# Kernel tuning notes

Measured on AMD Instinct MI355X. Metric: run time of the kernel, lower is better.

The kernel has to match this reference:

```python
import jax, jax.numpy as jnp
import numpy as np

IN_F = 1024
OUT_F = 1024
R = 16
NUM_USERS = 10000
NUM_ITEMS = 10000
BATCH = 4096
SCALING = 32.0 / 16.0  # lora_alpha / r


def setup_inputs() -> dict:
    key = jax.random.key(0)
    ks = jax.random.split(key, 9)
    return {
        "x": jax.random.normal(ks[0], (BATCH, IN_F), dtype=jnp.float32),
        "user_indices": jax.random.randint(ks[1], (BATCH,), 0, NUM_USERS, dtype=jnp.int32),
        "item_indices": jax.random.randint(ks[2], (BATCH,), 0, NUM_ITEMS, dtype=jnp.int32),
        "W_base": jax.random.normal(ks[3], (OUT_F, IN_F), dtype=jnp.float32) * 0.02,
        "b_base": jax.random.normal(ks[4], (OUT_F,), dtype=jnp.float32) * 0.02,
        "A": jax.random.normal(ks[5], (R, IN_F), dtype=jnp.float32) * 0.02,
        "B_user": jax.random.normal(ks[6], (NUM_USERS, OUT_F, R), dtype=jnp.float32) * 0.02,
        "B_item": jax.random.normal(ks[7], (NUM_ITEMS, OUT_F, R), dtype=jnp.float32) * 0.02,
        "W_common": jax.random.normal(ks[8], (OUT_F, R), dtype=jnp.float32) * 0.02,
    }


def reference(x, user_indices, item_indices, W_base, b_base, A, B_user, B_item, W_common):
    # base linear: [B, out]
    base = x @ W_base.T + b_base
    # lora_A (dropout p=0 -> identity): [B, r]
    a = x @ A.T
    # gather per-row LoRA-B matrices: [B, out, r]
    Bu = B_user[user_indices]
    Bi = B_item[item_indices]
    # batched low-rank matmuls + shared common projection
    user_part = jnp.einsum("bor,br->bo", Bu, a)
    item_part = jnp.einsum("bor,br->bo", Bi, a)
    common_part = a @ W_common.T
    return base + SCALING * (user_part + item_part + common_part)
```

## Files before the change

### kernel.cpp

```cpp
#include <hip/hip_runtime.h>
#include <hip/hip_bf16.h>
#include <cstdint>
#include <cstddef>

typedef __attribute__((ext_vector_type(8))) __bf16 bf16x8;
typedef __attribute__((ext_vector_type(4))) __bf16 bf16x4;
typedef __attribute__((ext_vector_type(4))) float f32x4;

#define BATCH 4096
#define IN_FEAT 1024
#define OUT_FEAT 1024
#define RNK 16
#define SCALE 2.0f

__global__ __launch_bounds__(256) void prep_kernel(
    const float* __restrict__ x, const float* __restrict__ A,
    const float* __restrict__ W,
    float* __restrict__ a_out, __bf16* __restrict__ x_bf,
    __bf16* __restrict__ w_bf)
{
    __shared__ float xs[IN_FEAT];
    const int b = blockIdx.x;
    const int t = threadIdx.x;

    if (b < OUT_FEAT) {
        const float4 wv = *reinterpret_cast<const float4*>(&W[(size_t)b * IN_FEAT + t * 4]);
        bf16x4 hw;
        hw[0] = (__bf16)wv.x; hw[1] = (__bf16)wv.y;
        hw[2] = (__bf16)wv.z; hw[3] = (__bf16)wv.w;
        *reinterpret_cast<bf16x4*>(&w_bf[(size_t)b * IN_FEAT + t * 4]) = hw;
    }

    const float4 v = *reinterpret_cast<const float4*>(&x[(size_t)b * IN_FEAT + t * 4]);
    xs[t * 4 + 0] = v.x; xs[t * 4 + 1] = v.y;
    xs[t * 4 + 2] = v.z; xs[t * 4 + 3] = v.w;
    bf16x4 h;
    h[0] = (__bf16)v.x; h[1] = (__bf16)v.y; h[2] = (__bf16)v.z; h[3] = (__bf16)v.w;
    *reinterpret_cast<bf16x4*>(&x_bf[(size_t)b * IN_FEAT + t * 4]) = h;
    __syncthreads();

    const int r = t >> 4;
    const int l16 = t & 15;
    const float* __restrict__ Ar = &A[r * IN_FEAT];
    float s = 0.f;
    #pragma unroll 8
    for (int j = 0; j < IN_FEAT / 16; ++j) {
        const int k = l16 + 16 * j;
        s += xs[k] * Ar[k];
    }
    s += __shfl_xor(s, 8);
    s += __shfl_xor(s, 4);
    s += __shfl_xor(s, 2);
    s += __shfl_xor(s, 1);
    if (l16 == 0) a_out[b * RNK + r] = s;
}

#define BM 64
#define BN 64
#define BK 64
#define LDK 72
#define CWS 20

__global__ __launch_bounds__(256) void fused_kernel(
    const __bf16* __restrict__ x_bf, const __bf16* __restrict__ w_bf,
    const float* __restrict__ a_buf,
    const int* __restrict__ uidx, const int* __restrict__ iidx,
    const float* __restrict__ b_base,
    const float* __restrict__ B_user, const float* __restrict__ B_item,
    const float* __restrict__ W_common,
    float* __restrict__ out)
{
    __shared__ __align__(16) __bf16 xs[BM * LDK];
    __shared__ __align__(16) __bf16 wsh[BN * LDK];
    __shared__ __align__(16) float a_s[BM * RNK];
    __shared__ __align__(16) float cw_s[BN * CWS];
    __shared__ float b_s[BN];
    __shared__ int u_s[BM];
    __shared__ int i_s[BM];

    const int t = threadIdx.x;

    const int bid = blockIdx.y * gridDim.x + blockIdx.x;
    const int nid = (bid & 7) * 128 + (bid >> 3);
    const int o0 = (nid & 15) * BN;
    const int b0 = (nid >> 4) * BM;

    if (t < BM) {
        u_s[t] = uidx[b0 + t];
        i_s[t] = iidx[b0 + t];
    }
    if (t < BN) b_s[t] = b_base[o0 + t];
    *reinterpret_cast<float4*>(&a_s[t * 4]) =
        *reinterpret_cast<const float4*>(&a_buf[(size_t)b0 * RNK + t * 4]);
    {
        const int row = t >> 2, col = (t & 3) * 4;
        const float4 v = *reinterpret_cast<const float4*>(
            &W_common[(size_t)(o0 + row) * RNK + col]);
        *reinterpret_cast<float4*>(&cw_s[row * CWS + col]) = v;
    }

    const int w  = t >> 6;
    const int wr = w >> 1;
    const int wc = w & 1;
    const int l  = t & 63;
    const int lr = l & 15;
    const int lg = l >> 4;

    const int srow  = t >> 2;
    const int skoff = (t & 3) * 16;

    f32x4 acc[2][2] = {};

    #pragma unroll
    for (int kt = 0; kt < IN_FEAT / BK; ++kt) {
        __syncthreads();
        {
            const uint4* g = reinterpret_cast<const uint4*>(
                &x_bf[(size_t)(b0 + srow) * IN_FEAT + kt * BK + skoff]);
            uint4 v0 = g[0], v1 = g[1];
            *reinterpret_cast<uint4*>(&xs[srow * LDK + skoff]) = v0;
            *reinterpret_cast<uint4*>(&xs[srow * LDK + skoff + 8]) = v1;
            const uint4* gw = reinterpret_cast<const uint4*>(
                &w_bf[(size_t)(o0 + srow) * IN_FEAT + kt * BK + skoff]);
            uint4 w0 = gw[0], w1 = gw[1];
            *reinterpret_cast<uint4*>(&wsh[srow * LDK + skoff]) = w0;
            *reinterpret_cast<uint4*>(&wsh[srow * LDK + skoff + 8]) = w1;
        }

        {
            const int nn = kt >> 3;
            const int mm = (kt >> 2) & 1;
            const int ii = kt & 3;
            const int ol = wc * 32 + nn * 16 + lr;
            const int o  = o0 + ol;
            const int bl = wr * 32 + mm * 16 + lg * 4 + ii;
            const size_t u  = (size_t)u_s[bl];
            const size_t iv = (size_t)i_s[bl];
            const float4* bu = reinterpret_cast<const float4*>(
                &B_user[(u * OUT_FEAT + (size_t)o) * RNK]);
            const float4* bi = reinterpret_cast<const float4*>(
                &B_item[(iv * OUT_FEAT + (size_t)o) * RNK]);
            const float4* av4 = reinterpret_cast<const float4*>(&a_s[bl * RNK]);
            const float4* cw4 = reinterpret_cast<const float4*>(&cw_s[ol * CWS]);
            float lora = 0.f;
            #pragma unroll
            for (int q = 0; q < 4; ++q) {
                const float4 cu = bu[q], ci = bi[q], aa = av4[q], cw = cw4[q];
                lora += (cu.x + ci.x + cw.x) * aa.x + (cu.y + ci.y + cw.y) * aa.y
                      + (cu.z + ci.z + cw.z) * aa.z + (cu.w + ci.w + cw.w) * aa.w;
            }
            acc[mm][nn][ii] += b_s[ol] + SCALE * lora;
        }
        __syncthreads();

        #pragma unroll
        for (int kk = 0; kk < BK; kk += 32) {
            bf16x8 af0 = *reinterpret_cast<const bf16x8*>(&xs[(wr * 32 + 0 * 16 + lr) * LDK + kk + lg * 8]);
            bf16x8 af1 = *reinterpret_cast<const bf16x8*>(&xs[(wr * 32 + 1 * 16 + lr) * LDK + kk + lg * 8]);
            bf16x8 bf0 = *reinterpret_cast<const bf16x8*>(&wsh[(wc * 32 + 0 * 16 + lr) * LDK + kk + lg * 8]);
            bf16x8 bf1 = *reinterpret_cast<const bf16x8*>(&wsh[(wc * 32 + 1 * 16 + lr) * LDK + kk + lg * 8]);
            acc[0][0] = __builtin_amdgcn_mfma_f32_16x16x32_bf16(af0, bf0, acc[0][0], 0, 0, 0);
            acc[0][1] = __builtin_amdgcn_mfma_f32_16x16x32_bf16(af0, bf1, acc[0][1], 0, 0, 0);
            acc[1][0] = __builtin_amdgcn_mfma_f32_16x16x32_bf16(af1, bf0, acc[1][0], 0, 0, 0);
            acc[1][1] = __builtin_amdgcn_mfma_f32_16x16x32_bf16(af1, bf1, acc[1][1], 0, 0, 0);
        }
    }

    #pragma unroll
    for (int n = 0; n < 2; ++n) {
        const int o = o0 + wc * 32 + n * 16 + lr;
        #pragma unroll
        for (int m = 0; m < 2; ++m) {
            #pragma unroll
            for (int i = 0; i < 4; ++i) {
                const int bl = wr * 32 + m * 16 + lg * 4 + i;
                out[(size_t)(b0 + bl) * OUT_FEAT + o] = acc[m][n][i];
            }
        }
    }
}

extern "C" void kernel_launch(void* const* d_in, const int* in_sizes, int n_in,
                              void* d_out, int out_size, void* d_ws, size_t ws_size,
                              hipStream_t stream) {
    const float* x        = (const float*)d_in[0];
    const int*   uidx     = (const int*)d_in[1];
    const int*   iidx     = (const int*)d_in[2];
    const float* W_base   = (const float*)d_in[3];
    const float* b_base   = (const float*)d_in[4];
    const float* A        = (const float*)d_in[5];
    const float* B_user   = (const float*)d_in[6];
    const float* B_item   = (const float*)d_in[7];
    const float* W_common = (const float*)d_in[8];
    float* out = (float*)d_out;

    float*  a_buf = (float*)d_ws;
    __bf16* x_bf  = (__bf16*)((char*)d_ws + (256 << 10));
    __bf16* w_bf  = (__bf16*)((char*)d_ws + (256 << 10) + (8 << 20));

    prep_kernel<<<BATCH, 256, 0, stream>>>(x, A, W_base, a_buf, x_bf, w_bf);

    dim3 grid(OUT_FEAT / BN, BATCH / BM);
    fused_kernel<<<grid, 256, 0, stream>>>(x_bf, w_bf, a_buf, uidx, iidx,
                                           b_base, B_user, B_item, W_common, out);
}
```

Before: 132.6 us.

## Fold W_common·A into base weight and software-pipeline gather and tile loads

The shared common projection is folded algebraically into the base weight (W_base + scale·W_common·A) in the prep kernel, so the fused kernel no longer loads or multiplies W_common. The main loop is restructured to prefetch the next K tile and the next B_user/B_item gather into registers before the barrier, which overlaps global latency with the MFMA work. The gather loads and output stores are marked nontemporal. In exchange, the folded weight is rounded to bf16, which slightly changes numerics, and register pressure rises.

```diff
diff --git a/kernel.cpp b/kernel.cpp
--- a/kernel.cpp
+++ b/kernel.cpp
@@ -15,28 +15,37 @@
 
 __global__ __launch_bounds__(256) void prep_kernel(
     const float* __restrict__ x, const float* __restrict__ A,
-    const float* __restrict__ W,
+    const float* __restrict__ W, const float* __restrict__ Wc,
     float* __restrict__ a_out, __bf16* __restrict__ x_bf,
     __bf16* __restrict__ w_bf)
 {
     __shared__ float xs[IN_FEAT];
     const int b = blockIdx.x;
     const int t = threadIdx.x;
+    const int k0 = t * 4;
 
     if (b < OUT_FEAT) {
-        const float4 wv = *reinterpret_cast<const float4*>(&W[(size_t)b * IN_FEAT + t * 4]);
+        float4 wv = *reinterpret_cast<const float4*>(&W[(size_t)b * IN_FEAT + k0]);
+        float cx = 0.f, cy = 0.f, cz = 0.f, cw = 0.f;
+        #pragma unroll
+        for (int r = 0; r < RNK; ++r) {
+            const float wcr = Wc[b * RNK + r];
+            const float4 av = *reinterpret_cast<const float4*>(&A[r * IN_FEAT + k0]);
+            cx += wcr * av.x; cy += wcr * av.y; cz += wcr * av.z; cw += wcr * av.w;
+        }
         bf16x4 hw;
-        hw[0] = (__bf16)wv.x; hw[1] = (__bf16)wv.y;
-        hw[2] = (__bf16)wv.z; hw[3] = (__bf16)wv.w;
-        *reinterpret_cast<bf16x4*>(&w_bf[(size_t)b * IN_FEAT + t * 4]) = hw;
-    }
-
-    const float4 v = *reinterpret_cast<const float4*>(&x[(size_t)b * IN_FEAT + t * 4]);
-    xs[t * 4 + 0] = v.x; xs[t * 4 + 1] = v.y;
-    xs[t * 4 + 2] = v.z; xs[t * 4 + 3] = v.w;
+        hw[0] = (__bf16)(wv.x + SCALE * cx);
+        hw[1] = (__bf16)(wv.y + SCALE * cy);
+        hw[2] = (__bf16)(wv.z + SCALE * cz);
+        hw[3] = (__bf16)(wv.w + SCALE * cw);
+        *reinterpret_cast<bf16x4*>(&w_bf[(size_t)b * IN_FEAT + k0]) = hw;
+    }
+
+    const float4 v = *reinterpret_cast<const float4*>(&x[(size_t)b * IN_FEAT + k0]);
+    xs[k0 + 0] = v.x; xs[k0 + 1] = v.y; xs[k0 + 2] = v.z; xs[k0 + 3] = v.w;
     bf16x4 h;
     h[0] = (__bf16)v.x; h[1] = (__bf16)v.y; h[2] = (__bf16)v.z; h[3] = (__bf16)v.w;
-    *reinterpret_cast<bf16x4*>(&x_bf[(size_t)b * IN_FEAT + t * 4]) = h;
+    *reinterpret_cast<bf16x4*>(&x_bf[(size_t)b * IN_FEAT + k0]) = h;
     __syncthreads();
 
     const int r = t >> 4;
@@ -59,7 +68,12 @@
 #define BN 64
 #define BK 64
 #define LDK 72
-#define CWS 20
+
+#define WG_BARRIER() do {                                        \
+    asm volatile("s_waitcnt lgkmcnt(0)" ::: "memory");           \
+    __builtin_amdgcn_s_barrier();                                \
+    asm volatile("" ::: "memory");                               \
+} while (0)
 
 __global__ __launch_bounds__(256) void fused_kernel(
     const __bf16* __restrict__ x_bf, const __bf16* __restrict__ w_bf,
@@ -67,13 +81,11 @@
     const int* __restrict__ uidx, const int* __restrict__ iidx,
     const float* __restrict__ b_base,
     const float* __restrict__ B_user, const float* __restrict__ B_item,
-    const float* __restrict__ W_common,
     float* __restrict__ out)
 {
     __shared__ __align__(16) __bf16 xs[BM * LDK];
     __shared__ __align__(16) __bf16 wsh[BN * LDK];
     __shared__ __align__(16) float a_s[BM * RNK];
-    __shared__ __align__(16) float cw_s[BN * CWS];
     __shared__ float b_s[BN];
     __shared__ int u_s[BM];
     __shared__ int i_s[BM];
@@ -92,12 +104,6 @@
     if (t < BN) b_s[t] = b_base[o0 + t];
     *reinterpret_cast<float4*>(&a_s[t * 4]) =
         *reinterpret_cast<const float4*>(&a_buf[(size_t)b0 * RNK + t * 4]);
-    {
-        const int row = t >> 2, col = (t & 3) * 4;
-        const float4 v = *reinterpret_cast<const float4*>(
-            &W_common[(size_t)(o0 + row) * RNK + col]);
-        *reinterpret_cast<float4*>(&cw_s[row * CWS + col]) = v;
-    }
 
     const int w  = t >> 6;
     const int wr = w >> 1;
@@ -110,59 +116,87 @@
     const int skoff = (t & 3) * 16;
 
     f32x4 acc[2][2] = {};
+    uint4 sx0, sx1, sw0, sw1;
+    f32x4 gu[4], gi[4];
+
+    #define STAGE_LOAD(kt) do {                                                      \
+        const __bf16* px_ = &x_bf[(size_t)(b0 + srow) * IN_FEAT + (kt) * BK + skoff];\
+        sx0 = *reinterpret_cast<const uint4*>(px_);                                  \
+        sx1 = *reinterpret_cast<const uint4*>(px_ + 8);                              \
+        const __bf16* pw_ = &w_bf[(size_t)(o0 + srow) * IN_FEAT + (kt) * BK + skoff];\
+        sw0 = *reinterpret_cast<const uint4*>(pw_);                                  \
+        sw1 = *reinterpret_cast<const uint4*>(pw_ + 8);                              \
+    } while (0)
+
+    #define STAGE_WRITE() do {                                                      \
+        *reinterpret_cast<uint4*>(&xs[srow * LDK + skoff])      = sx0;               \
+        *reinterpret_cast<uint4*>(&xs[srow * LDK + skoff + 8])  = sx1;               \
+        *reinterpret_cast<uint4*>(&wsh[srow * LDK + skoff])     = sw0;               \
+        *reinterpret_cast<uint4*>(&wsh[srow * LDK + skoff + 8]) = sw1;               \
+    } while (0)
+
+    #define GATHER_ISSUE(s) do {                                                    \
+        const int nn_ = (s) >> 3, mm_ = ((s) >> 2) & 1, ii_ = (s) & 3;               \
+        const int ol_ = wc * 32 + nn_ * 16 + lr;                                     \
+        const int bl_ = wr * 32 + mm_ * 16 + lg * 4 + ii_;                           \
+        const f32x4* pu_ = reinterpret_cast<const f32x4*>(                           \
+            &B_user[((size_t)u_s[bl_] * OUT_FEAT + (size_t)(o0 + ol_)) * RNK]);      \
+        const f32x4* pi_ = reinterpret_cast<const f32x4*>(                           \
+            &B_item[((size_t)i_s[bl_] * OUT_FEAT + (size_t)(o0 + ol_)) * RNK]);      \
+        gu[0] = __builtin_nontemporal_load(pu_ + 0);                                 \
+        gu[1] = __builtin_nontemporal_load(pu_ + 1);                                 \
+        gu[2] = __builtin_nontemporal_load(pu_ + 2);                                 \
+        gu[3] = __builtin_nontemporal_load(pu_ + 3);                                 \
+        gi[0] = __builtin_nontemporal_load(pi_ + 0);                                 \
+        gi[1] = __builtin_nontemporal_load(pi_ + 1);                                 \
+        gi[2] = __builtin_nontemporal_load(pi_ + 2);                                 \
+        gi[3] = __builtin_nontemporal_load(pi_ + 3);                                 \
+    } while (0)
+
+    #define GATHER_CONSUME(s) do {                                                  \
+        const int nn_ = (s) >> 3, mm_ = ((s) >> 2) & 1, ii_ = (s) & 3;               \
+        const int ol_ = wc * 32 + nn_ * 16 + lr;                                     \
+        const int bl_ = wr * 32 + mm_ * 16 + lg * 4 + ii_;                           \
+        const f32x4* av4_ = reinterpret_cast<const f32x4*>(&a_s[bl_ * RNK]);         \
+        float lora_ = 0.f;                                                           \
+        _Pragma("unroll")                                                            \
+        for (int q = 0; q < 4; ++q) {                                                \
+            const f32x4 aa_ = av4_[q];                                               \
+            const f32x4 su_ = gu[q] + gi[q];                                         \
+            lora_ += su_[0] * aa_[0] + su_[1] * aa_[1]                               \
+                   + su_[2] * aa_[2] + su_[3] * aa_[3];                              \
+        }                                                                            \
+        acc[mm_][nn_][ii_] += b_s[ol_] + SCALE * lora_;                              \
+    } while (0)
+
+    STAGE_LOAD(0);
+    WG_BARRIER();
+    GATHER_ISSUE(0);
+    STAGE_WRITE();
+    WG_BARRIER();
 
     #pragma unroll
     for (int kt = 0; kt < IN_FEAT / BK; ++kt) {
-        __syncthreads();
-        {
-            const uint4* g = reinterpret_cast<const uint4*>(
-                &x_bf[(size_t)(b0 + srow) * IN_FEAT + kt * BK + skoff]);
-            uint4 v0 = g[0], v1 = g[1];
-            *reinterpret_cast<uint4*>(&xs[srow * LDK + skoff]) = v0;
-            *reinterpret_cast<uint4*>(&xs[srow * LDK + skoff + 8]) = v1;
-            const uint4* gw = reinterpret_cast<const uint4*>(
-                &w_bf[(size_t)(o0 + srow) * IN_FEAT + kt * BK + skoff]);
-            uint4 w0 = gw[0], w1 = gw[1];
-            *reinterpret_cast<uint4*>(&wsh[srow * LDK + skoff]) = w0;
-            *reinterpret_cast<uint4*>(&wsh[srow * LDK + skoff + 8]) = w1;
-        }
-
-        {
-            const int nn = kt >> 3;
-            const int mm = (kt >> 2) & 1;
-            const int ii = kt & 3;
-            const int ol = wc * 32 + nn * 16 + lr;
-            const int o  = o0 + ol;
-            const int bl = wr * 32 + mm * 16 + lg * 4 + ii;
-            const size_t u  = (size_t)u_s[bl];
-            const size_t iv = (size_t)i_s[bl];
-            const float4* bu = reinterpret_cast<const float4*>(
-                &B_user[(u * OUT_FEAT + (size_t)o) * RNK]);
-            const float4* bi = reinterpret_cast<const float4*>(
-                &B_item[(iv * OUT_FEAT + (size_t)o) * RNK]);
-            const float4* av4 = reinterpret_cast<const float4*>(&a_s[bl * RNK]);
-            const float4* cw4 = reinterpret_cast<const float4*>(&cw_s[ol * CWS]);
-            float lora = 0.f;
-            #pragma unroll
-            for (int q = 0; q < 4; ++q) {
-                const float4 cu = bu[q], ci = bi[q], aa = av4[q], cw = cw4[q];
-                lora += (cu.x + ci.x + cw.x) * aa.x + (cu.y + ci.y + cw.y) * aa.y
-                      + (cu.z + ci.z + cw.z) * aa.z + (cu.w + ci.w + cw.w) * aa.w;
-            }
-            acc[mm][nn][ii] += b_s[ol] + SCALE * lora;
-        }
-        __syncthreads();
-
         #pragma unroll
         for (int kk = 0; kk < BK; kk += 32) {
-            bf16x8 af0 = *reinterpret_cast<const bf16x8*>(&xs[(wr * 32 + 0 * 16 + lr) * LDK + kk + lg * 8]);
-            bf16x8 af1 = *reinterpret_cast<const bf16x8*>(&xs[(wr * 32 + 1 * 16 + lr) * LDK + kk + lg * 8]);
-            bf16x8 bf0 = *reinterpret_cast<const bf16x8*>(&wsh[(wc * 32 + 0 * 16 + lr) * LDK + kk + lg * 8]);
-            bf16x8 bf1 = *reinterpret_cast<const bf16x8*>(&wsh[(wc * 32 + 1 * 16 + lr) * LDK + kk + lg * 8]);
+            bf16x8 af0 = *reinterpret_cast<const bf16x8*>(&xs[(wr * 32 + 0 + lr) * LDK + kk + lg * 8]);
+            bf16x8 af1 = *reinterpret_cast<const bf16x8*>(&xs[(wr * 32 + 16 + lr) * LDK + kk + lg * 8]);
+            bf16x8 bf0 = *reinterpret_cast<const bf16x8*>(&wsh[(wc * 32 + 0 + lr) * LDK + kk + lg * 8]);
+            bf16x8 bf1 = *reinterpret_cast<const bf16x8*>(&wsh[(wc * 32 + 16 + lr) * LDK + kk + lg * 8]);
             acc[0][0] = __builtin_amdgcn_mfma_f32_16x16x32_bf16(af0, bf0, acc[0][0], 0, 0, 0);
             acc[0][1] = __builtin_amdgcn_mfma_f32_16x16x32_bf16(af0, bf1, acc[0][1], 0, 0, 0);
             acc[1][0] = __builtin_amdgcn_mfma_f32_16x16x32_bf16(af1, bf0, acc[1][0], 0, 0, 0);
             acc[1][1] = __builtin_amdgcn_mfma_f32_16x16x32_bf16(af1, bf1, acc[1][1], 0, 0, 0);
+        }
+
+        GATHER_CONSUME(kt);
+
+        if (kt < IN_FEAT / BK - 1) {
+            STAGE_LOAD(kt + 1);
+            GATHER_ISSUE(kt + 1);
+            WG_BARRIER();
+            STAGE_WRITE();
+            WG_BARRIER();
         }
     }
 
@@ -174,10 +208,16 @@
             #pragma unroll
             for (int i = 0; i < 4; ++i) {
                 const int bl = wr * 32 + m * 16 + lg * 4 + i;
-                out[(size_t)(b0 + bl) * OUT_FEAT + o] = acc[m][n][i];
+                __builtin_nontemporal_store(acc[m][n][i],
+                    &out[(size_t)(b0 + bl) * OUT_FEAT + o]);
             }
         }
     }
+
+    #undef STAGE_LOAD
+    #undef STAGE_WRITE
+    #undef GATHER_ISSUE
+    #undef GATHER_CONSUME
 }
 
 extern "C" void kernel_launch(void* const* d_in, const int* in_sizes, int n_in,
@@ -198,9 +238,9 @@
     __bf16* x_bf  = (__bf16*)((char*)d_ws + (256 << 10));
     __bf16* w_bf  = (__bf16*)((char*)d_ws + (256 << 10) + (8 << 20));
 
-    prep_kernel<<<BATCH, 256, 0, stream>>>(x, A, W_base, a_buf, x_bf, w_bf);
+    prep_kernel<<<BATCH, 256, 0, stream>>>(x, A, W_base, W_common, a_buf, x_bf, w_bf);
 
     dim3 grid(OUT_FEAT / BN, BATCH / BM);
     fused_kernel<<<grid, 256, 0, stream>>>(x_bf, w_bf, a_buf, uidx, iidx,
-                                           b_base, B_user, B_item, W_common, out);
+                                           b_base, B_user, B_item, out);
 }
```

Measured after the change: 206.6 us. +55.8%, slower.
